# Kernel optimization log

Hardware: AMD Instinct MI355X
Metric: run time of the kernel (lower is better)

## Reference

```python
import jax, jax.numpy as jnp
import numpy as np

D = 512      # d_model
H = 8        # n_heads
DH = D // H  # d_head
WIN = 128    # window radius
FF = 4 * D   # ffn hidden
B, T = 4, 2048
EPS = 1e-5


def _ln(x, g, b):
    mu = jnp.mean(x, axis=-1, keepdims=True)
    var = jnp.mean((x - mu) ** 2, axis=-1, keepdims=True)
    return (x - mu) * jax.lax.rsqrt(var + EPS) * g + b


def _rope(x):
    # standard rotate-half RoPE over the full d_model dim (applied to ln(x)
    # before q/k/v projections, as in the source module)
    t, d = x.shape[-2], x.shape[-1]
    half = d // 2
    inv_freq = 1.0 / (10000.0 ** (jnp.arange(half, dtype=jnp.float32) / half))
    ang = jnp.arange(t, dtype=jnp.float32)[:, None] * inv_freq[None, :]  # (T, half)
    cos, sin = jnp.cos(ang), jnp.sin(ang)
    x1, x2 = x[..., :half], x[..., half:]
    return jnp.concatenate([x1 * cos - x2 * sin, x1 * sin + x2 * cos], axis=-1)


def setup_inputs() -> dict:
    key = jax.random.key(0)
    ks = jax.random.split(key, 16)
    s = 0.02
    inp = {
        "x": jax.random.normal(ks[0], (B, T, D), dtype=jnp.float32),
        "Wq": jax.random.normal(ks[1], (D, D), dtype=jnp.float32) * s,
        "bq": jnp.zeros((D,), jnp.float32),
        "Wk": jax.random.normal(ks[2], (D, D), dtype=jnp.float32) * s,
        "bk": jnp.zeros((D,), jnp.float32),
        "Wv": jax.random.normal(ks[3], (D, D), dtype=jnp.float32) * s,
        "bv": jnp.zeros((D,), jnp.float32),
        "Wo": jax.random.normal(ks[4], (D, D), dtype=jnp.float32) * s,
        "bo": jnp.zeros((D,), jnp.float32),
        "ln_g": jnp.ones((D,), jnp.float32),
        "ln_b": jnp.zeros((D,), jnp.float32),
        "ffln_g": jnp.ones((D,), jnp.float32),
        "ffln_b": jnp.zeros((D,), jnp.float32),
        "W1": jax.random.normal(ks[5], (D, FF), dtype=jnp.float32) * s,
        "b1": jnp.zeros((FF,), jnp.float32),
        "W2": jax.random.normal(ks[6], (FF, D), dtype=jnp.float32) * s,
        "b2": jnp.zeros((D,), jnp.float32),
    }
    return inp


def reference(x, Wq, bq, Wk, bk, Wv, bv, Wo, bo, ln_g, ln_b, ffln_g, ffln_b, W1, b1, W2, b2):
    b, t, d = x.shape
    h = _rope(_ln(x, ln_g, ln_b))
    q = (h @ Wq + bq).reshape(b, t, H, DH).transpose(0, 2, 1, 3)  # (B,H,T,DH)
    k = (h @ Wk + bk).reshape(b, t, H, DH).transpose(0, 2, 1, 3)
    v = (h @ Wv + bv).reshape(b, t, H, DH).transpose(0, 2, 1, 3)

    scores = jnp.einsum("bhqd,bhkd->bhqk", q, k) / jnp.sqrt(jnp.float32(DH))
    # Faithful to source local_mask semantics under torch SDPA bool-mask
    # convention (True = attend): attention is ALLOWED where |i-j| > window.
    idx = jnp.arange(t)
    allowed = jnp.abs(idx[:, None] - idx[None, :]) > WIN  # (T,T) bool
    scores = jnp.where(allowed, scores, -jnp.inf)
    attn = jax.nn.softmax(scores, axis=-1)
    o = jnp.einsum("bhqk,bhkd->bhqd", attn, v)
    o = o.transpose(0, 2, 1, 3).reshape(b, t, d)
    x = x + (o @ Wo + bo)

    # source applies self.ln AND the ff's internal LayerNorm back-to-back
    f = _ln(_ln(x, ln_g, ln_b), ffln_g, ffln_b)
    f = jax.nn.gelu(f @ W1 + b1, approximate=False) @ W2 + b2
    return x + f
```

## Files before the change

### kernel.cpp

```cpp
#include <hip/hip_runtime.h>
#include <cmath>

typedef __bf16 bf16x8 __attribute__((ext_vector_type(8)));
typedef float  f32x4  __attribute__((ext_vector_type(4)));
typedef float  f32x16 __attribute__((ext_vector_type(16)));

#define MFMA(a, b, c)   __builtin_amdgcn_mfma_f32_16x16x32_bf16((a), (b), (c), 0, 0, 0)
#define MFMA32(a, b, c) __builtin_amdgcn_mfma_f32_32x32x16_bf16((a), (b), (c), 0, 0, 0)

static __device__ __forceinline__ __bf16 f2bf(float f) {
  union { float f; unsigned u; } v; v.f = f;
  unsigned r = v.u + 0x7fffu + ((v.u >> 16) & 1u);
  union { unsigned short u; __bf16 b; } o; o.u = (unsigned short)(r >> 16);
  return o.b;
}

typedef const __attribute__((address_space(1))) void* gas_t;
typedef __attribute__((address_space(3))) void* las_t;
static __device__ __forceinline__ void load_lds16(const __bf16* g, __bf16* l) {
  __builtin_amdgcn_global_load_lds((gas_t)g, (las_t)l, 16, 0, 0);
}

__global__ __launch_bounds__(256) void k_transpose_all(
    const float* __restrict__ Wq, const float* __restrict__ Wk,
    const float* __restrict__ Wv, const float* __restrict__ Wo,
    const float* __restrict__ W1, const float* __restrict__ W2,
    __bf16* __restrict__ wqkv, __bf16* __restrict__ wo,
    __bf16* __restrict__ w1t, __bf16* __restrict__ w2t) {
  int idx = blockIdx.x * 256 + threadIdx.x;
  const float* src; __bf16* dst; int off, logK, N;
  if (idx < 1048576) {
    int which = idx >> 18; off = idx & 262143; logK = 9; N = 512;
    src = which == 0 ? Wq : which == 1 ? Wk : which == 2 ? Wv : Wo;
    dst = which < 3 ? wqkv + which * 262144 : wo;
  } else if (idx < 2097152) {
    off = idx - 1048576; logK = 9; N = 2048; src = W1; dst = w1t;
  } else {
    off = idx - 2097152; logK = 11; N = 512; src = W2; dst = w2t;
  }
  int n = off >> logK, k = off & ((1 << logK) - 1);
  dst[off] = f2bf(src[(size_t)k * N + n]);
}

__global__ __launch_bounds__(256) void k_ln_rope(const float* __restrict__ x,
                                                 const float* __restrict__ g,
                                                 const float* __restrict__ b,
                                                 __bf16* __restrict__ h) {
  int n = blockIdx.x, tid = threadIdx.x;
  const float* row = x + (size_t)n * 512;
  float v1 = row[tid], v2 = row[tid + 256];
  float s = v1 + v2, ss = v1 * v1 + v2 * v2;
  #pragma unroll
  for (int off = 1; off < 64; off <<= 1) { s += __shfl_xor(s, off, 64); ss += __shfl_xor(ss, off, 64); }
  __shared__ float red[2][4];
  if ((tid & 63) == 0) { red[0][tid >> 6] = s; red[1][tid >> 6] = ss; }
  __syncthreads();
  s  = red[0][0] + red[0][1] + red[0][2] + red[0][3];
  ss = red[1][0] + red[1][1] + red[1][2] + red[1][3];
  float mu = s * (1.f / 512.f);
  float var = ss * (1.f / 512.f) - mu * mu;
  float rs = rsqrtf(var + 1e-5f);
  float y1 = (v1 - mu) * rs * g[tid] + b[tid];
  float y2 = (v2 - mu) * rs * g[tid + 256] + b[tid + 256];
  int t = n & 2047;
  float inv = __expf(-(float)tid * 0.03597789207803197f);
  float ang = (float)t * inv;
  float sn, c;
  __sincosf(ang, &sn, &c);
  h[(size_t)n * 512 + tid]       = f2bf(y1 * c - y2 * sn);
  h[(size_t)n * 512 + tid + 256] = f2bf(y1 * sn + y2 * c);
}

template <int K>
static __device__ __forceinline__ void gemm128(const __bf16* __restrict__ A,
                                               const __bf16* __restrict__ Bt,
                                               f32x4 (&acc)[4][4]) {
  __shared__ __bf16 lA[128 * 32];
  __shared__ __bf16 lB[128 * 32];
  int bm = blockIdx.x & 63, bn = blockIdx.x >> 6;
  int tid = threadIdx.x, w = tid >> 6, lane = tid & 63;
  int l16 = lane & 15, quad = lane >> 4;
  int wr = (w >> 1) * 64, wc = (w & 1) * 64;
  const __bf16* ga = A  + (size_t)(bm * 128 + w * 32 + (lane >> 2)) * K + (lane & 3) * 8;
  const __bf16* gb = Bt + (size_t)(bn * 128 + w * 32 + (lane >> 2)) * K + (lane & 3) * 8;
  __bf16* sa = lA + w * 1024;
  __bf16* sb = lB + w * 1024;
  #pragma unroll
  for (int i = 0; i < 4; ++i)
    #pragma unroll
    for (int j = 0; j < 4; ++j) acc[i][j] = {0.f, 0.f, 0.f, 0.f};
  const size_t rstep = (size_t)16 * K;
  for (int k0 = 0; k0 < K; k0 += 32) {
    load_lds16(ga + k0,         sa);
    load_lds16(ga + k0 + rstep, sa + 512);
    load_lds16(gb + k0,         sb);
    load_lds16(gb + k0 + rstep, sb + 512);
    __syncthreads();
    bf16x8 af[4], bfr[4];
    #pragma unroll
    for (int i = 0; i < 4; ++i) af[i]  = *(const bf16x8*)&lA[(wr + i * 16 + l16) * 32 + quad * 8];
    #pragma unroll
    for (int j = 0; j < 4; ++j) bfr[j] = *(const bf16x8*)&lB[(wc + j * 16 + l16) * 32 + quad * 8];
    #pragma unroll
    for (int i = 0; i < 4; ++i)
      #pragma unroll
      for (int j = 0; j < 4; ++j) acc[i][j] = MFMA(af[i], bfr[j], acc[i][j]);
    __syncthreads();
  }
}

#define G128_EPILOG_IDX                                 \
  int bm = blockIdx.x & 63, bn = blockIdx.x >> 6;       \
  int lane = threadIdx.x & 63, w = threadIdx.x >> 6;    \
  int l16 = lane & 15, quad = lane >> 4;                \
  int wr = (w >> 1) * 64, wc = (w & 1) * 64;

__global__ __launch_bounds__(256) void k_gemm_qkv(const __bf16* __restrict__ A,
                                                  const __bf16* __restrict__ Bt,
                                                  const float* __restrict__ bq,
                                                  const float* __restrict__ bk,
                                                  const float* __restrict__ bv,
                                                  __bf16* __restrict__ qo,
                                                  __bf16* __restrict__ ko,
                                                  __bf16* __restrict__ vT) {
  f32x4 acc[4][4];
  gemm128<512>(A, Bt, acc);
  G128_EPILOG_IDX
  int proj = bn >> 2;
  const float* bias = proj == 0 ? bq : (proj == 1 ? bk : bv);
  float scale = proj == 0 ? 0.125f : 1.f;
  if (proj < 2) {
    __bf16* dst = proj == 0 ? qo : ko;
    #pragma unroll
    for (int i = 0; i < 4; ++i)
      #pragma unroll
      for (int j = 0; j < 4; ++j)
        #pragma unroll
        for (int r = 0; r < 4; ++r) {
          int c = (bn * 128 + wc + j * 16 + l16) & 511;
          int m = bm * 128 + wr + i * 16 + quad * 4 + r;
          int bI = m >> 11, t = m & 2047;
          int head = c >> 6, dh = c & 63;
          dst[(((size_t)bI * 8 + head) * 2048 + t) * 64 + dh] = f2bf((acc[i][j][r] + bias[c]) * scale);
        }
  } else {
    #pragma unroll
    for (int i = 0; i < 4; ++i)
      #pragma unroll
      for (int j = 0; j < 4; ++j)
        #pragma unroll
        for (int r = 0; r < 4; ++r) {
          int c = (bn * 128 + wc + j * 16 + l16) & 511;
          int m = bm * 128 + wr + i * 16 + quad * 4 + r;
          int bI = m >> 11, t = m & 2047;
          int head = c >> 6, dh = c & 63;
          vT[(((size_t)bI * 8 + head) * 64 + dh) * 2048 + t] = f2bf(acc[i][j][r] + bias[c]);
        }
  }
}

__global__ __launch_bounds__(512) void k_attn(const __bf16* __restrict__ q,
                                              const __bf16* __restrict__ k,
                                              const __bf16* __restrict__ vT,
                                              __bf16* __restrict__ o) {
  __shared__ __align__(16) __bf16 Kt[32 * 64];
  __shared__ __align__(16) __bf16 Vt[64 * 32];
  __shared__ __align__(16) __bf16 P[8][32][40];
  __shared__ float cbuf[4][64][17];
  int bh = blockIdx.x >> 4, qblk = blockIdx.x & 15;
  int tid = threadIdx.x, w = tid >> 6, lane = tid & 63;
  int l32 = lane & 31, h32 = lane >> 5;
  int qw = w & 3, half = w >> 2;
  int qB = qblk * 128;
  int q0 = qB + qw * 32;
  const __bf16* qb = q + (size_t)bh * 2048 * 64;
  const __bf16* kb = k + (size_t)bh * 2048 * 64;
  const __bf16* vb = vT + (size_t)bh * 64 * 2048;
  bf16x8 aq[4];
  #pragma unroll
  for (int i = 0; i < 4; ++i)
    aq[i] = *(const bf16x8*)(qb + (size_t)(q0 + l32) * 64 + i * 16 + h32 * 8);
  f32x16 on0 = {0,0,0,0,0,0,0,0,0,0,0,0,0,0,0,0};
  f32x16 on1 = {0,0,0,0,0,0,0,0,0,0,0,0,0,0,0,0};
  float lsum[16];
  #pragma unroll
  for (int i = 0; i < 16; ++i) lsum[i] = 0.f;
  const __bf16* gstage; __bf16* sdst; int stagemul;
  if (w < 4) {
    int row = w * 8 + (lane >> 3);
    gstage = kb + (size_t)row * 64 + (((lane & 7) ^ (row & 7)) * 8);
    sdst = Kt + w * 512; stagemul = 64;
  } else {
    int row = (w - 4) * 16 + (lane >> 2);
    gstage = vb + (size_t)row * 2048 + (((lane & 3) ^ (row & 3)) * 8);
    sdst = Vt + (w - 4) * 512; stagemul = 1;
  }

  for (int it = 0; it < 64; ++it) {
    int kt0 = it * 32;
    if ((unsigned)(kt0 - qB) <= 96u) continue;
    load_lds16(gstage + (size_t)kt0 * stagemul, sdst);
    __syncthreads();
    bool mywork = ((it & 1) == half) && !((q0 + 31 - kt0 <= 128) && (kt0 + 31 - q0 <= 128));
    if (mywork) {
      bool need_mask = !((kt0 >= q0 + 160) || (kt0 + 31 <= q0 - 129));
      f32x16 sc = {0,0,0,0,0,0,0,0,0,0,0,0,0,0,0,0};
      #pragma unroll
      for (int i = 0; i < 4; ++i) {
        bf16x8 bk;
        __builtin_memcpy(&bk, &Kt[l32 * 64 + ((((i << 1) | h32) ^ (l32 & 7)) * 8)], 16);
        sc = MFMA32(aq[i], bk, sc);
      }
      #pragma unroll
      for (int reg = 0; reg < 16; ++reg) {
        int row = (reg & 3) + 8 * (reg >> 2) + 4 * h32;
        float p = __expf(sc[reg]);
        if (need_mask) {
          int qi = q0 + row, kj = kt0 + l32;
          if ((unsigned)(qi - kj + 128) <= 256u) p = 0.f;
        }
        P[w][row][l32] = f2bf(p);
        lsum[reg] += p;
      }
      bf16x8 ap0, ap1;
      __builtin_memcpy(&ap0, &P[w][l32][h32 * 8], 16);
      __builtin_memcpy(&ap1, &P[w][l32][16 + h32 * 8], 16);
      #pragma unroll
      for (int kk = 0; kk < 2; ++kk) {
        bf16x8 ap = kk ? ap1 : ap0;
        bf16x8 bv0, bv1;
        int c0 = ((kk * 2 + h32) ^ (l32 & 3)) * 8;
        __builtin_memcpy(&bv0, &Vt[l32 * 32 + c0], 16);
        __builtin_memcpy(&bv1, &Vt[(32 + l32) * 32 + c0], 16);
        on0 = MFMA32(ap, bv0, on0);
        on1 = MFMA32(ap, bv1, on1);
      }
    }
    __syncthreads();
  }
  if (half) {
    for (int i = 0; i < 16; ++i) cbuf[qw][lane][i] = on0[i];
  }
  __syncthreads();
  if (!half) {
    for (int i = 0; i < 16; ++i) on0[i] += cbuf[qw][lane][i];
  }
  __syncthreads();
  if (half) {
    for (int i = 0; i < 16; ++i) cbuf[qw][lane][i] = on1[i];
  }
  __syncthreads();
  if (!half) {
    for (int i = 0; i < 16; ++i) on1[i] += cbuf[qw][lane][i];
  }
  __syncthreads();
  if (half) {
    for (int i = 0; i < 16; ++i) cbuf[qw][lane][i] = lsum[i];
  }
  __syncthreads();
  if (!half) {
    #pragma unroll
    for (int i = 0; i < 16; ++i) {
      float s = lsum[i] + cbuf[qw][lane][i];
      #pragma unroll
      for (int off = 1; off < 32; off <<= 1) s += __shfl_xor(s, off, 64);
      lsum[i] = 1.f / s;
    }
    int bI = bh >> 3, head = bh & 7;
    #pragma unroll
    for (int reg = 0; reg < 16; ++reg) {
      int row = (reg & 3) + 8 * (reg >> 2) + 4 * h32;
      size_t base = ((size_t)(bI * 2048 + q0 + row)) * 512 + head * 64;
      o[base + l32]      = f2bf(on0[reg] * lsum[reg]);
      o[base + 32 + l32] = f2bf(on1[reg] * lsum[reg]);
    }
  }
}

__global__ __launch_bounds__(256) void k_gemm_oproj(const __bf16* __restrict__ A,
                                                    const __bf16* __restrict__ Bt,
                                                    const float* __restrict__ bo,
                                                    const float* __restrict__ xin,
                                                    float* __restrict__ x2) {
  f32x4 acc[4][4];
  gemm128<512>(A, Bt, acc);
  G128_EPILOG_IDX
  #pragma unroll
  for (int i = 0; i < 4; ++i)
    #pragma unroll
    for (int j = 0; j < 4; ++j)
      #pragma unroll
      for (int r = 0; r < 4; ++r) {
        int n = bn * 128 + wc + j * 16 + l16;
        int m = bm * 128 + wr + i * 16 + quad * 4 + r;
        size_t idx = (size_t)m * 512 + n;
        x2[idx] = xin[idx] + acc[i][j][r] + bo[n];
      }
}

__global__ __launch_bounds__(256) void k_ln_ln(const float* __restrict__ x2,
                                               const float* __restrict__ g1v,
                                               const float* __restrict__ b1v,
                                               const float* __restrict__ g2v,
                                               const float* __restrict__ b2v,
                                               __bf16* __restrict__ fout) {
  int n = blockIdx.x, tid = threadIdx.x;
  const float* row = x2 + (size_t)n * 512;
  float v1 = row[tid], v2 = row[tid + 256];
  __shared__ float red[2][4];
  float s = v1 + v2, ss = v1 * v1 + v2 * v2;
  #pragma unroll
  for (int off = 1; off < 64; off <<= 1) { s += __shfl_xor(s, off, 64); ss += __shfl_xor(ss, off, 64); }
  if ((tid & 63) == 0) { red[0][tid >> 6] = s; red[1][tid >> 6] = ss; }
  __syncthreads();
  s  = red[0][0] + red[0][1] + red[0][2] + red[0][3];
  ss = red[1][0] + red[1][1] + red[1][2] + red[1][3];
  float mu = s * (1.f / 512.f), var = ss * (1.f / 512.f) - mu * mu;
  float rs = rsqrtf(var + 1e-5f);
  float y1 = (v1 - mu) * rs * g1v[tid] + b1v[tid];
  float y2 = (v2 - mu) * rs * g1v[tid + 256] + b1v[tid + 256];
  __syncthreads();
  s = y1 + y2; ss = y1 * y1 + y2 * y2;
  #pragma unroll
  for (int off = 1; off < 64; off <<= 1) { s += __shfl_xor(s, off, 64); ss += __shfl_xor(ss, off, 64); }
  if ((tid & 63) == 0) { red[0][tid >> 6] = s; red[1][tid >> 6] = ss; }
  __syncthreads();
  s  = red[0][0] + red[0][1] + red[0][2] + red[0][3];
  ss = red[1][0] + red[1][1] + red[1][2] + red[1][3];
  float mu2 = s * (1.f / 512.f), var2 = ss * (1.f / 512.f) - mu2 * mu2;
  float rs2 = rsqrtf(var2 + 1e-5f);
  fout[(size_t)n * 512 + tid]       = f2bf((y1 - mu2) * rs2 * g2v[tid] + b2v[tid]);
  fout[(size_t)n * 512 + tid + 256] = f2bf((y2 - mu2) * rs2 * g2v[tid + 256] + b2v[tid + 256]);
}

__global__ __launch_bounds__(256) void k_gemm_ffn1(const __bf16* __restrict__ A,
                                                   const __bf16* __restrict__ Bt,
                                                   const float* __restrict__ b1,
                                                   __bf16* __restrict__ g1) {
  f32x4 acc[4][4];
  gemm128<512>(A, Bt, acc);
  G128_EPILOG_IDX
  #pragma unroll
  for (int i = 0; i < 4; ++i)
    #pragma unroll
    for (int j = 0; j < 4; ++j)
      #pragma unroll
      for (int r = 0; r < 4; ++r) {
        int n = bn * 128 + wc + j * 16 + l16;
        int m = bm * 128 + wr + i * 16 + quad * 4 + r;
        float t = acc[i][j][r] + b1[n];
        float ge = 0.5f * t * (1.f + erff(t * 0.7071067811865475f));
        g1[(size_t)m * 2048 + n] = f2bf(ge);
      }
}

__global__ __launch_bounds__(256) void k_gemm_ffn2(const __bf16* __restrict__ A,
                                                   const __bf16* __restrict__ Bt,
                                                   const float* __restrict__ b2,
                                                   const float* __restrict__ x2,
                                                   float* __restrict__ out) {
  f32x4 acc[4][4];
  gemm128<2048>(A, Bt, acc);
  G128_EPILOG_IDX
  #pragma unroll
  for (int i = 0; i < 4; ++i)
    #pragma unroll
    for (int j = 0; j < 4; ++j)
      #pragma unroll
      for (int r = 0; r < 4; ++r) {
        int n = bn * 128 + wc + j * 16 + l16;
        int m = bm * 128 + wr + i * 16 + quad * 4 + r;
        size_t idx = (size_t)m * 512 + n;
        out[idx] = x2[idx] + acc[i][j][r] + b2[n];
      }
}

extern "C" void kernel_launch(void* const* d_in, const int* in_sizes, int n_in,
                              void* d_out, int out_size, void* d_ws, size_t ws_size,
                              hipStream_t stream) {
  (void)in_sizes; (void)n_in; (void)out_size; (void)ws_size;
  const float* x   = (const float*)d_in[0];
  const float* Wq  = (const float*)d_in[1];
  const float* bq  = (const float*)d_in[2];
  const float* Wk  = (const float*)d_in[3];
  const float* bk  = (const float*)d_in[4];
  const float* Wv  = (const float*)d_in[5];
  const float* bv  = (const float*)d_in[6];
  const float* Wo  = (const float*)d_in[7];
  const float* bo  = (const float*)d_in[8];
  const float* lng = (const float*)d_in[9];
  const float* lnb = (const float*)d_in[10];
  const float* ffg = (const float*)d_in[11];
  const float* ffb = (const float*)d_in[12];
  const float* W1  = (const float*)d_in[13];
  const float* b1  = (const float*)d_in[14];
  const float* W2  = (const float*)d_in[15];
  const float* b2  = (const float*)d_in[16];
  float* out = (float*)d_out;

  char* ws = (char*)d_ws;
  __bf16* h    = (__bf16*)(ws);
  __bf16* qb   = (__bf16*)(ws + (size_t)8 * 1024 * 1024);
  __bf16* kb   = (__bf16*)(ws + (size_t)16 * 1024 * 1024);
  __bf16* vT   = (__bf16*)(ws + (size_t)24 * 1024 * 1024);
  float*  x2   = (float*)(ws + (size_t)32 * 1024 * 1024);
  __bf16* fb   = (__bf16*)(ws + (size_t)48 * 1024 * 1024);
  __bf16* wqkv = (__bf16*)(ws + (size_t)56 * 1024 * 1024);
  __bf16* wo   = wqkv + 3 * 512 * 512;
  __bf16* w1t  = wo + 512 * 512;
  __bf16* w2t  = w1t + 512 * 2048;
  __bf16* g1   = (__bf16*)(ws);

  k_transpose_all<<<12288, 256, 0, stream>>>(Wq, Wk, Wv, Wo, W1, W2, wqkv, wo, w1t, w2t);
  k_ln_rope<<<8192, 256, 0, stream>>>(x, lng, lnb, h);
  k_gemm_qkv<<<64 * 12, 256, 0, stream>>>(h, wqkv, bq, bk, bv, qb, kb, vT);
  k_attn<<<32 * 16, 512, 0, stream>>>(qb, kb, vT, h);
  k_gemm_oproj<<<64 * 4, 256, 0, stream>>>(h, wo, bo, x, x2);
  k_ln_ln<<<8192, 256, 0, stream>>>(x2, lng, lnb, ffg, ffb, fb);
  k_gemm_ffn1<<<64 * 16, 256, 0, stream>>>(fb, w1t, b1, g1);
  k_gemm_ffn2<<<64 * 4, 256, 0, stream>>>(g1, w2t, b2, x2, out);
}
```

Measured before the change: 330.0 us.

## Widen GEMM and attention K-tiles to 64 with XOR-swizzled LDS and 8 waves

```diff
diff --git a/kernel.cpp b/kernel.cpp
--- a/kernel.cpp
+++ b/kernel.cpp
@@ -74,37 +74,49 @@
 template <int K>
 static __device__ __forceinline__ void gemm128(const __bf16* __restrict__ A,
                                                const __bf16* __restrict__ Bt,
-                                               f32x4 (&acc)[4][4]) {
-  __shared__ __bf16 lA[128 * 32];
-  __shared__ __bf16 lB[128 * 32];
+                                               f32x4 (&acc)[2][4]) {
+  __shared__ __bf16 lA[128 * 64];
+  __shared__ __bf16 lB[128 * 64];
   int bm = blockIdx.x & 63, bn = blockIdx.x >> 6;
   int tid = threadIdx.x, w = tid >> 6, lane = tid & 63;
   int l16 = lane & 15, quad = lane >> 4;
-  int wr = (w >> 1) * 64, wc = (w & 1) * 64;
-  const __bf16* ga = A  + (size_t)(bm * 128 + w * 32 + (lane >> 2)) * K + (lane & 3) * 8;
-  const __bf16* gb = Bt + (size_t)(bn * 128 + w * 32 + (lane >> 2)) * K + (lane & 3) * 8;
-  __bf16* sa = lA + w * 1024;
-  __bf16* sb = lB + w * 1024;
-  #pragma unroll
-  for (int i = 0; i < 4; ++i)
+  int wr = (w & 3) * 32, wc = (w >> 2) * 64;
+  int srow = w * 8 + (lane >> 3);
+  int sg = (lane & 7) ^ (srow & 7);
+  const __bf16* ga = A  + (size_t)(bm * 128 + srow) * K + sg * 8;
+  const __bf16* gb = Bt + (size_t)(bn * 128 + srow) * K + sg * 8;
+  __bf16* saw = lA + w * 512;
+  __bf16* sbw = lB + w * 512;
+  #pragma unroll
+  for (int i = 0; i < 2; ++i)
     #pragma unroll
     for (int j = 0; j < 4; ++j) acc[i][j] = {0.f, 0.f, 0.f, 0.f};
-  const size_t rstep = (size_t)16 * K;
-  for (int k0 = 0; k0 < K; k0 += 32) {
-    load_lds16(ga + k0,         sa);
-    load_lds16(ga + k0 + rstep, sa + 512);
-    load_lds16(gb + k0,         sb);
-    load_lds16(gb + k0 + rstep, sb + 512);
+  const size_t rstep = (size_t)64 * K;
+  for (int k0 = 0; k0 < K; k0 += 64) {
+    load_lds16(ga + k0,         saw);
+    load_lds16(ga + k0 + rstep, saw + 4096);
+    load_lds16(gb + k0,         sbw);
+    load_lds16(gb + k0 + rstep, sbw + 4096);
     __syncthreads();
-    bf16x8 af[4], bfr[4];
-    #pragma unroll
-    for (int i = 0; i < 4; ++i) af[i]  = *(const bf16x8*)&lA[(wr + i * 16 + l16) * 32 + quad * 8];
-    #pragma unroll
-    for (int j = 0; j < 4; ++j) bfr[j] = *(const bf16x8*)&lB[(wc + j * 16 + l16) * 32 + quad * 8];
-    #pragma unroll
-    for (int i = 0; i < 4; ++i)
-      #pragma unroll
-      for (int j = 0; j < 4; ++j) acc[i][j] = MFMA(af[i], bfr[j], acc[i][j]);
+    #pragma unroll
+    for (int kk = 0; kk < 2; ++kk) {
+      int gg = kk * 4 + quad;
+      bf16x8 af[2], bfr[4];
+      #pragma unroll
+      for (int i = 0; i < 2; ++i) {
+        int row = wr + i * 16 + l16;
+        __builtin_memcpy(&af[i], &lA[row * 64 + ((gg ^ (row & 7)) * 8)], 16);
+      }
+      #pragma unroll
+      for (int j = 0; j < 4; ++j) {
+        int row = wc + j * 16 + l16;
+        __builtin_memcpy(&bfr[j], &lB[row * 64 + ((gg ^ (row & 7)) * 8)], 16);
+      }
+      #pragma unroll
+      for (int i = 0; i < 2; ++i)
+        #pragma unroll
+        for (int j = 0; j < 4; ++j) acc[i][j] = MFMA(af[i], bfr[j], acc[i][j]);
+    }
     __syncthreads();
   }
 }
@@ -113,9 +125,9 @@
   int bm = blockIdx.x & 63, bn = blockIdx.x >> 6;       \
   int lane = threadIdx.x & 63, w = threadIdx.x >> 6;    \
   int l16 = lane & 15, quad = lane >> 4;                \
-  int wr = (w >> 1) * 64, wc = (w & 1) * 64;
-
-__global__ __launch_bounds__(256) void k_gemm_qkv(const __bf16* __restrict__ A,
+  int wr = (w & 3) * 32, wc = (w >> 2) * 64;
+
+__global__ __launch_bounds__(512) void k_gemm_qkv(const __bf16* __restrict__ A,
                                                   const __bf16* __restrict__ Bt,
                                                   const float* __restrict__ bq,
                                                   const float* __restrict__ bk,
@@ -123,7 +135,7 @@
                                                   __bf16* __restrict__ qo,
                                                   __bf16* __restrict__ ko,
                                                   __bf16* __restrict__ vT) {
-  f32x4 acc[4][4];
+  f32x4 acc[2][4];
   gemm128<512>(A, Bt, acc);
   G128_EPILOG_IDX
   int proj = bn >> 2;
@@ -132,7 +144,7 @@
   if (proj < 2) {
     __bf16* dst = proj == 0 ? qo : ko;
     #pragma unroll
-    for (int i = 0; i < 4; ++i)
+    for (int i = 0; i < 2; ++i)
       #pragma unroll
       for (int j = 0; j < 4; ++j)
         #pragma unroll
@@ -145,7 +157,7 @@
         }
   } else {
     #pragma unroll
-    for (int i = 0; i < 4; ++i)
+    for (int i = 0; i < 2; ++i)
       #pragma unroll
       for (int j = 0; j < 4; ++j)
         #pragma unroll
@@ -163,14 +175,14 @@
                                               const __bf16* __restrict__ k,
                                               const __bf16* __restrict__ vT,
                                               __bf16* __restrict__ o) {
-  __shared__ __align__(16) __bf16 Kt[32 * 64];
-  __shared__ __align__(16) __bf16 Vt[64 * 32];
+  __shared__ __align__(16) __bf16 Kt[64 * 64];
+  __shared__ __align__(16) __bf16 Vt[64 * 64];
   __shared__ __align__(16) __bf16 P[8][32][40];
   __shared__ float cbuf[4][64][17];
   int bh = blockIdx.x >> 4, qblk = blockIdx.x & 15;
   int tid = threadIdx.x, w = tid >> 6, lane = tid & 63;
   int l32 = lane & 31, h32 = lane >> 5;
-  int qw = w & 3, half = w >> 2;
+  int qw = w & 3, half = w >> 2, hoff = half * 32;
   int qB = qblk * 128;
   int q0 = qB + qw * 32;
   const __bf16* qb = q + (size_t)bh * 2048 * 64;
@@ -185,30 +197,30 @@
   float lsum[16];
   #pragma unroll
   for (int i = 0; i < 16; ++i) lsum[i] = 0.f;
-  const __bf16* gstage; __bf16* sdst; int stagemul;
-  if (w < 4) {
-    int row = w * 8 + (lane >> 3);
-    gstage = kb + (size_t)row * 64 + (((lane & 7) ^ (row & 7)) * 8);
-    sdst = Kt + w * 512; stagemul = 64;
-  } else {
-    int row = (w - 4) * 16 + (lane >> 2);
-    gstage = vb + (size_t)row * 2048 + (((lane & 3) ^ (row & 3)) * 8);
-    sdst = Vt + (w - 4) * 512; stagemul = 1;
-  }
-
-  for (int it = 0; it < 64; ++it) {
-    int kt0 = it * 32;
-    if ((unsigned)(kt0 - qB) <= 96u) continue;
-    load_lds16(gstage + (size_t)kt0 * stagemul, sdst);
+  int srow = w * 8 + (lane >> 3);
+  int sg = (lane & 7) ^ (srow & 7);
+  const __bf16* gk = kb + (size_t)srow * 64 + sg * 8;
+  const __bf16* gv = vb + (size_t)srow * 2048 + sg * 8;
+  __bf16* skw = Kt + w * 512;
+  __bf16* svw = Vt + w * 512;
+
+  for (int it = 0; it < 32; ++it) {
+    int kt64 = it * 64;
+    if ((unsigned)(kt64 - qB) <= 64u) continue;
+    load_lds16(gk + (size_t)kt64 * 64, skw);
+    load_lds16(gv + kt64, svw);
     __syncthreads();
-    bool mywork = ((it & 1) == half) && !((q0 + 31 - kt0 <= 128) && (kt0 + 31 - q0 <= 128));
-    if (mywork) {
-      bool need_mask = !((kt0 >= q0 + 160) || (kt0 + 31 <= q0 - 129));
+    int myk0 = kt64 + hoff;
+    bool skip = (q0 + 31 - myk0 <= 128) && (myk0 + 31 - q0 <= 128);
+    if (!skip) {
+      bool need_mask = !((myk0 >= q0 + 160) || (myk0 <= q0 - 160));
       f32x16 sc = {0,0,0,0,0,0,0,0,0,0,0,0,0,0,0,0};
+      int krow = hoff + l32;
       #pragma unroll
       for (int i = 0; i < 4; ++i) {
+        int gg = i * 2 + h32;
         bf16x8 bk;
-        __builtin_memcpy(&bk, &Kt[l32 * 64 + ((((i << 1) | h32) ^ (l32 & 7)) * 8)], 16);
+        __builtin_memcpy(&bk, &Kt[krow * 64 + ((gg ^ (l32 & 7)) * 8)], 16);
         sc = MFMA32(aq[i], bk, sc);
       }
       #pragma unroll
@@ -216,7 +228,7 @@
         int row = (reg & 3) + 8 * (reg >> 2) + 4 * h32;
         float p = __expf(sc[reg]);
         if (need_mask) {
-          int qi = q0 + row, kj = kt0 + l32;
+          int qi = q0 + row, kj = myk0 + l32;
           if ((unsigned)(qi - kj + 128) <= 256u) p = 0.f;
         }
         P[w][row][l32] = f2bf(p);
@@ -228,10 +240,10 @@
       #pragma unroll
       for (int kk = 0; kk < 2; ++kk) {
         bf16x8 ap = kk ? ap1 : ap0;
+        int gg = half * 4 + kk * 2 + h32;
         bf16x8 bv0, bv1;
-        int c0 = ((kk * 2 + h32) ^ (l32 & 3)) * 8;
-        __builtin_memcpy(&bv0, &Vt[l32 * 32 + c0], 16);
-        __builtin_memcpy(&bv1, &Vt[(32 + l32) * 32 + c0], 16);
+        __builtin_memcpy(&bv0, &Vt[l32 * 64 + ((gg ^ (l32 & 7)) * 8)], 16);
+        __builtin_memcpy(&bv1, &Vt[(32 + l32) * 64 + ((gg ^ (l32 & 7)) * 8)], 16);
         on0 = MFMA32(ap, bv0, on0);
         on1 = MFMA32(ap, bv1, on1);
       }
@@ -277,16 +289,16 @@
   }
 }
 
-__global__ __launch_bounds__(256) void k_gemm_oproj(const __bf16* __restrict__ A,
+__global__ __launch_bounds__(512) void k_gemm_oproj(const __bf16* __restrict__ A,
                                                     const __bf16* __restrict__ Bt,
                                                     const float* __restrict__ bo,
                                                     const float* __restrict__ xin,
                                                     float* __restrict__ x2) {
-  f32x4 acc[4][4];
+  f32x4 acc[2][4];
   gemm128<512>(A, Bt, acc);
   G128_EPILOG_IDX
   #pragma unroll
-  for (int i = 0; i < 4; ++i)
+  for (int i = 0; i < 2; ++i)
     #pragma unroll
     for (int j = 0; j < 4; ++j)
       #pragma unroll
@@ -333,15 +345,15 @@
   fout[(size_t)n * 512 + tid + 256] = f2bf((y2 - mu2) * rs2 * g2v[tid + 256] + b2v[tid + 256]);
 }
 
-__global__ __launch_bounds__(256) void k_gemm_ffn1(const __bf16* __restrict__ A,
+__global__ __launch_bounds__(512) void k_gemm_ffn1(const __bf16* __restrict__ A,
                                                    const __bf16* __restrict__ Bt,
                                                    const float* __restrict__ b1,
                                                    __bf16* __restrict__ g1) {
-  f32x4 acc[4][4];
+  f32x4 acc[2][4];
   gemm128<512>(A, Bt, acc);
   G128_EPILOG_IDX
   #pragma unroll
-  for (int i = 0; i < 4; ++i)
+  for (int i = 0; i < 2; ++i)
     #pragma unroll
     for (int j = 0; j < 4; ++j)
       #pragma unroll
@@ -354,16 +366,16 @@
       }
 }
 
-__global__ __launch_bounds__(256) void k_gemm_ffn2(const __bf16* __restrict__ A,
+__global__ __launch_bounds__(512) void k_gemm_ffn2(const __bf16* __restrict__ A,
                                                    const __bf16* __restrict__ Bt,
                                                    const float* __restrict__ b2,
                                                    const float* __restrict__ x2,
                                                    float* __restrict__ out) {
-  f32x4 acc[4][4];
+  f32x4 acc[2][4];
   gemm128<2048>(A, Bt, acc);
   G128_EPILOG_IDX
   #pragma unroll
-  for (int i = 0; i < 4; ++i)
+  for (int i = 0; i < 2; ++i)
     #pragma unroll
     for (int j = 0; j < 4; ++j)
       #pragma unroll
@@ -413,10 +425,10 @@
 
   k_transpose_all<<<12288, 256, 0, stream>>>(Wq, Wk, Wv, Wo, W1, W2, wqkv, wo, w1t, w2t);
   k_ln_rope<<<8192, 256, 0, stream>>>(x, lng, lnb, h);
-  k_gemm_qkv<<<64 * 12, 256, 0, stream>>>(h, wqkv, bq, bk, bv, qb, kb, vT);
+  k_gemm_qkv<<<64 * 12, 512, 0, stream>>>(h, wqkv, bq, bk, bv, qb, kb, vT);
   k_attn<<<32 * 16, 512, 0, stream>>>(qb, kb, vT, h);
-  k_gemm_oproj<<<64 * 4, 256, 0, stream>>>(h, wo, bo, x, x2);
+  k_gemm_oproj<<<64 * 4, 512, 0, stream>>>(h, wo, bo, x, x2);
   k_ln_ln<<<8192, 256, 0, stream>>>(x2, lng, lnb, ffg, ffb, fb);
-  k_gemm_ffn1<<<64 * 16, 256, 0, stream>>>(fb, w1t, b1, g1);
-  k_gemm_ffn2<<<64 * 4, 256, 0, stream>>>(g1, w2t, b2, x2, out);
-}
+  k_gemm_ffn1<<<64 * 16, 512, 0, stream>>>(fb, w1t, b1, g1);
+  k_gemm_ffn2<<<64 * 4, 512, 0, stream>>>(g1, w2t, b2, x2, out);
+}
```

Result: faster. 287.1 us (-13.0%).
